# Performance work log

Measured on AMD Instinct MI355X. Metric: run time of the kernel, lower is better.

## Reference

```python
import jax, jax.numpy as jnp
import numpy as np

IN_DIM = 2048
OUT_DIM = 2048
GRID_SIZE = 8
BATCH = 4096
LN_EPS = 1e-5


def setup_inputs() -> dict:
    key = jax.random.key(0)
    k_x, k_w = jax.random.split(key)
    x = jax.random.normal(k_x, (BATCH, IN_DIM), dtype=jnp.float32)
    spline_weight = jax.random.normal(k_w, (OUT_DIM, IN_DIM, GRID_SIZE), dtype=jnp.float32) * 0.1
    return {
        "x": x,
        "ln_weight": jnp.ones((IN_DIM,), jnp.float32),
        "ln_bias": jnp.zeros((IN_DIM,), jnp.float32),
        "spline_weight": spline_weight,
        "scale_base": jnp.ones((OUT_DIM, IN_DIM), jnp.float32),
        "bias": jnp.zeros((OUT_DIM,), jnp.float32),
        "rbf_beta": jnp.full((1,), 2.0, jnp.float32),
        "grid": jnp.linspace(-1.0, 1.0, GRID_SIZE, dtype=jnp.float32),
    }


def reference(x, ln_weight, ln_bias, spline_weight, scale_base, bias, rbf_beta, grid):
    # LayerNorm over last dim (eps=1e-5, elementwise affine)
    mu = jnp.mean(x, axis=-1, keepdims=True)
    var = jnp.mean(jnp.square(x - mu), axis=-1, keepdims=True)
    xn = (x - mu) * jax.lax.rsqrt(var + LN_EPS) * ln_weight + ln_bias  # (B, in)

    beta = jnp.clip(rbf_beta, 0.5, 6.0)  # (1,)
    # RBF basis: (B, in, G)
    basis = jnp.exp(-jnp.square(xn[..., None] - grid) * beta)

    # Torch einsum('bdig,oid->bod') broadcasts the singleton d of basis against
    # spline_weight's last axis and sums g; after .sum(-1) this equals
    # (sum_g basis) @ (sum_d spline_weight).T
    S = basis.sum(-1)              # (B, in)
    Wd = spline_weight.sum(-1)     # (out, in)
    spline_sum = jnp.einsum('bi,oi->bo', S, Wd)

    base_out = jnp.einsum('bi,oi->bo', xn, scale_base)
    return base_out + spline_sum + bias
```

## Files before the change

kernel.cpp:

```cpp
#include <hip/hip_runtime.h>
#include <hip/hip_bf16.h>
#include <stdint.h>

constexpr int IN_DIM   = 2048;
constexpr int OUT_DIM  = 2048;
constexpr int BATCH    = 4096;
constexpr int KDIM     = 2 * IN_DIM;
constexpr float LN_EPS = 1e-5f;

#define TILE 128
#define BK   64
constexpr int NK    = KDIM / BK;
constexpr int STAGE = TILE * BK;

typedef __attribute__((ext_vector_type(8))) short  short8;
typedef __attribute__((ext_vector_type(4))) float  f32x4;

__device__ __forceinline__ unsigned short f2bf(float f) {
  __hip_bfloat16 h = __float2bfloat16(f);
  return *reinterpret_cast<unsigned short*>(&h);
}
__device__ __forceinline__ unsigned pack2bf(float a, float b) {
  return (unsigned)f2bf(a) | ((unsigned)f2bf(b) << 16);
}

__global__ __launch_bounds__(256) void ln_rbf_kernel(
    const float* __restrict__ x, const float* __restrict__ lnw,
    const float* __restrict__ lnb, const float* __restrict__ betap,
    const float* __restrict__ grid, unsigned short* __restrict__ A)
{
  const int row = blockIdx.x;
  const int tid = threadIdx.x;
  const float4* xr = reinterpret_cast<const float4*>(x + (size_t)row * IN_DIM);
  float4 v0 = xr[tid];
  float4 v1 = xr[tid + 256];
  float s = (v0.x + v0.y) + (v0.z + v0.w) + (v1.x + v1.y) + (v1.z + v1.w);
  float q = v0.x * v0.x + v0.y * v0.y + v0.z * v0.z + v0.w * v0.w
          + v1.x * v1.x + v1.y * v1.y + v1.z * v1.z + v1.w * v1.w;
  #pragma unroll
  for (int off = 32; off > 0; off >>= 1) {
    s += __shfl_down(s, off, 64);
    q += __shfl_down(q, off, 64);
  }
  __shared__ float red[10];
  const int lane = tid & 63, wv = tid >> 6;
  if (lane == 0) { red[wv] = s; red[4 + wv] = q; }
  __syncthreads();
  if (tid == 0) {
    float ts = (red[0] + red[1]) + (red[2] + red[3]);
    float tq = (red[4] + red[5]) + (red[6] + red[7]);
    float mu  = ts * (1.0f / IN_DIM);
    float var = tq * (1.0f / IN_DIM) - mu * mu;
    red[8] = mu;
    red[9] = rsqrtf(var + LN_EPS);
  }
  __syncthreads();
  const float mu = red[8], rs = red[9];
  const float beta = fminf(fmaxf(betap[0], 0.5f), 6.0f);
  float g[8];
  #pragma unroll
  for (int i = 0; i < 8; i++) g[i] = grid[i];
  const float4* w4 = reinterpret_cast<const float4*>(lnw);
  const float4* b4 = reinterpret_cast<const float4*>(lnb);
  unsigned short* Ar = A + (size_t)row * KDIM;
  #pragma unroll
  for (int h = 0; h < 2; h++) {
    const int idx = tid + h * 256;
    float4 xv  = (h == 0) ? v0 : v1;
    float4 wv4 = w4[idx];
    float4 bv4 = b4[idx];
    float xa[4] = {xv.x, xv.y, xv.z, xv.w};
    float wa[4] = {wv4.x, wv4.y, wv4.z, wv4.w};
    float ba[4] = {bv4.x, bv4.y, bv4.z, bv4.w};
    float xn[4], S[4];
    #pragma unroll
    for (int c = 0; c < 4; c++) {
      float xnv = (xa[c] - mu) * rs * wa[c] + ba[c];
      xn[c] = xnv;
      float acc = 0.f;
      #pragma unroll
      for (int gg = 0; gg < 8; gg++) {
        float d = xnv - g[gg];
        acc += __expf(-beta * d * d);
      }
      S[c] = acc;
    }
    uint2 px, ps;
    px.x = pack2bf(xn[0], xn[1]);
    px.y = pack2bf(xn[2], xn[3]);
    ps.x = pack2bf(S[0], S[1]);
    ps.y = pack2bf(S[2], S[3]);
    *reinterpret_cast<uint2*>(Ar + idx * 4) = px;
    *reinterpret_cast<uint2*>(Ar + IN_DIM + idx * 4) = ps;
  }
}

constexpr int SW_F4   = OUT_DIM * IN_DIM * 2;
constexpr int SB_F4   = OUT_DIM * IN_DIM / 4;

__global__ __launch_bounds__(256) void pack_b_kernel(
    const float* __restrict__ sw, const float* __restrict__ sb,
    unsigned* __restrict__ Bu)
{
  const int g = blockIdx.x * 256 + threadIdx.x;
  const int lane = threadIdx.x & 63;
  if (g < SW_F4) {
    float4 v = reinterpret_cast<const float4*>(sw)[g];
    float s = (v.x + v.y) + (v.z + v.w);
    s += __shfl_xor(s, 1, 64);
    float hi = __shfl_down(s, 2, 64);
    if ((lane & 3) == 0) {
      const int i_lin = g >> 1;
      const int o = i_lin >> 11;
      const int i = i_lin & (IN_DIM - 1);
      Bu[(size_t)o * (KDIM / 2) + (IN_DIM / 2) + (i >> 1)] = pack2bf(s, hi);
    }
  } else {
    const int t = g - SW_F4;
    float4 v = reinterpret_cast<const float4*>(sb)[t];
    const int o  = t >> 9;
    const int i4 = t & 511;
    uint2 u;
    u.x = pack2bf(v.x, v.y);
    u.y = pack2bf(v.z, v.w);
    *reinterpret_cast<uint2*>(&Bu[(size_t)o * (KDIM / 2) + i4 * 2]) = u;
  }
}

__device__ __forceinline__ void gld_lds16(const unsigned short* g, unsigned short* l) {
  __builtin_amdgcn_global_load_lds(
      (const __attribute__((address_space(1))) void*)g,
      (__attribute__((address_space(3))) void*)l, 16, 0, 0);
}

__global__ __launch_bounds__(256) void gemm_kernel(
    const unsigned short* __restrict__ A, const unsigned short* __restrict__ Bm,
    const float* __restrict__ bias, float* __restrict__ out)
{
  __shared__ __align__(16) unsigned short As[2 * STAGE];
  __shared__ __align__(16) unsigned short Bs[2 * STAGE];
  const int tid  = threadIdx.x;
  const int lane = tid & 63;
  const int wv   = tid >> 6;
  const int wr   = wv >> 1;
  const int wc   = wv & 1;
  const int m0   = blockIdx.y * TILE;
  const int n0   = blockIdx.x * TILE;
  const int lrow = lane & 15;
  const int lkq  = lane >> 4;

  f32x4 acc[4][4] = {};

  const unsigned short* Ap[4];
  const unsigned short* Bp[4];
  unsigned short* ldsA[4];
  unsigned short* ldsB[4];
  #pragma unroll
  for (int j = 0; j < 4; j++) {
    const int seg  = j * 256 + wv * 64 + lane;
    const int row  = seg >> 3;
    const int gcol = ((seg & 7) ^ (row & 7)) * 8;
    Ap[j] = A  + (size_t)(m0 + row) * KDIM + gcol;
    Bp[j] = Bm + (size_t)(n0 + row) * KDIM + gcol;
    ldsA[j] = &As[(j * 256 + wv * 64) * 8];
    ldsB[j] = &Bs[(j * 256 + wv * 64) * 8];
  }

  #pragma unroll
  for (int j = 0; j < 4; j++) gld_lds16(Ap[j], ldsA[j]);
  #pragma unroll
  for (int j = 0; j < 4; j++) gld_lds16(Bp[j], ldsB[j]);

  #pragma unroll 1
  for (int kt = 0; kt < NK; kt++) {
    __syncthreads();
    const int cur = (kt & 1) * STAGE;
    if (kt + 1 < NK) {
      const int nxt = ((kt + 1) & 1) * STAGE;
      const int koff = (kt + 1) * BK;
      #pragma unroll
      for (int j = 0; j < 4; j++) gld_lds16(Ap[j] + koff, ldsA[j] + nxt);
      #pragma unroll
      for (int j = 0; j < 4; j++) gld_lds16(Bp[j] + koff, ldsB[j] + nxt);
    }

    short8 af[2][4], bf[2][4];
    #pragma unroll
    for (int h = 0; h < 2; h++) {
      #pragma unroll
      for (int mi = 0; mi < 4; mi++) {
        const int r = wr * 64 + mi * 16 + lrow;
        af[h][mi] = *reinterpret_cast<const short8*>(
            &As[cur + r * BK + (((h << 2) | lkq) ^ (lrow & 7)) * 8]);
      }
      #pragma unroll
      for (int ni = 0; ni < 4; ni++) {
        const int r = wc * 64 + ni * 16 + lrow;
        bf[h][ni] = *reinterpret_cast<const short8*>(
            &Bs[cur + r * BK + (((h << 2) | lkq) ^ (lrow & 7)) * 8]);
      }
    }
    #pragma unroll
    for (int h = 0; h < 2; h++)
      #pragma unroll
      for (int mi = 0; mi < 4; mi++)
        #pragma unroll
        for (int ni = 0; ni < 4; ni++)
          acc[mi][ni] = __builtin_amdgcn_mfma_f32_16x16x32_bf16(
              af[h][mi], bf[h][ni], acc[mi][ni], 0, 0, 0);
  }

  const int rb = (lane >> 4) * 4;
  #pragma unroll
  for (int ni = 0; ni < 4; ni++) {
    const int col = n0 + wc * 64 + ni * 16 + lrow;
    const float bv = bias[col];
    #pragma unroll
    for (int mi = 0; mi < 4; mi++) {
      const int rowm = m0 + wr * 64 + mi * 16 + rb;
      #pragma unroll
      for (int r = 0; r < 4; r++)
        out[(size_t)(rowm + r) * OUT_DIM + col] = acc[mi][ni][r] + bv;
    }
  }
}

extern "C" void kernel_launch(void* const* d_in, const int* in_sizes, int n_in,
                              void* d_out, int out_size, void* d_ws, size_t ws_size,
                              hipStream_t stream) {
  const float* x    = (const float*)d_in[0];
  const float* lnw  = (const float*)d_in[1];
  const float* lnb  = (const float*)d_in[2];
  const float* sw   = (const float*)d_in[3];
  const float* sb   = (const float*)d_in[4];
  const float* bias = (const float*)d_in[5];
  const float* beta = (const float*)d_in[6];
  const float* grid = (const float*)d_in[7];
  float* out = (float*)d_out;

  unsigned short* A = (unsigned short*)d_ws;
  unsigned short* B = A + (size_t)BATCH * KDIM;

  hipLaunchKernelGGL(ln_rbf_kernel, dim3(BATCH), dim3(256), 0, stream,
                     x, lnw, lnb, beta, grid, A);
  hipLaunchKernelGGL(pack_b_kernel, dim3((SW_F4 + SB_F4) / 256), dim3(256), 0, stream,
                     sw, sb, (unsigned*)B);
  hipLaunchKernelGGL(gemm_kernel, dim3(OUT_DIM / TILE, BATCH / TILE), dim3(256), 0, stream,
                     A, B, bias, out);
}
```

Measured before the change: 311.9 us.

## Split GEMM into producer and consumer waves synchronised through LDS atomic counters

```diff
diff --git a/kernel.cpp b/kernel.cpp
--- a/kernel.cpp
+++ b/kernel.cpp
@@ -133,56 +133,75 @@
       (__attribute__((address_space(3))) void*)l, 16, 0, 0);
 }
 
-__global__ __launch_bounds__(256) void gemm_kernel(
+__global__ __launch_bounds__(512) void gemm_kernel(
     const unsigned short* __restrict__ A, const unsigned short* __restrict__ Bm,
     const float* __restrict__ bias, float* __restrict__ out)
 {
   __shared__ __align__(16) unsigned short As[2 * STAGE];
   __shared__ __align__(16) unsigned short Bs[2 * STAGE];
+  __shared__ unsigned prod_done, cons_done;
+
   const int tid  = threadIdx.x;
   const int lane = tid & 63;
   const int wv   = tid >> 6;
+  const int m0   = blockIdx.y * TILE;
+  const int n0   = blockIdx.x * TILE;
+
+  if (tid == 0) { prod_done = 0u; cons_done = 0u; }
+  __syncthreads();
+
+  if (wv >= 4) {
+    const int p = wv - 4;
+    const unsigned short* Ap[4];
+    const unsigned short* Bp[4];
+    unsigned short* lA[4];
+    unsigned short* lB[4];
+    #pragma unroll
+    for (int j = 0; j < 4; j++) {
+      const int seg  = j * 256 + p * 64 + lane;
+      const int row  = seg >> 3;
+      const int gcol = ((seg & 7) ^ (row & 7)) * 8;
+      Ap[j] = A  + (size_t)(m0 + row) * KDIM + gcol;
+      Bp[j] = Bm + (size_t)(n0 + row) * KDIM + gcol;
+      lA[j] = &As[(j * 256 + p * 64) * 8];
+      lB[j] = &Bs[(j * 256 + p * 64) * 8];
+    }
+    #pragma unroll 1
+    for (int kt = 0; kt < NK; kt++) {
+      if (kt >= 2) {
+        const unsigned need = 4u * (unsigned)(kt - 1);
+        while (__hip_atomic_load(&cons_done, __ATOMIC_ACQUIRE,
+                                 __HIP_MEMORY_SCOPE_WORKGROUP) < need)
+          __builtin_amdgcn_s_sleep(1);
+      }
+      const int slot = (kt & 1) * STAGE;
+      const int koff = kt * BK;
+      #pragma unroll
+      for (int j = 0; j < 4; j++) gld_lds16(Ap[j] + koff, lA[j] + slot);
+      #pragma unroll
+      for (int j = 0; j < 4; j++) gld_lds16(Bp[j] + koff, lB[j] + slot);
+      __builtin_amdgcn_s_waitcnt(0);
+      if (lane == 0)
+        __hip_atomic_fetch_add(&prod_done, 1u, __ATOMIC_RELEASE,
+                               __HIP_MEMORY_SCOPE_WORKGROUP);
+    }
+    return;
+  }
+
   const int wr   = wv >> 1;
   const int wc   = wv & 1;
-  const int m0   = blockIdx.y * TILE;
-  const int n0   = blockIdx.x * TILE;
   const int lrow = lane & 15;
   const int lkq  = lane >> 4;
 
   f32x4 acc[4][4] = {};
 
-  const unsigned short* Ap[4];
-  const unsigned short* Bp[4];
-  unsigned short* ldsA[4];
-  unsigned short* ldsB[4];
-  #pragma unroll
-  for (int j = 0; j < 4; j++) {
-    const int seg  = j * 256 + wv * 64 + lane;
-    const int row  = seg >> 3;
-    const int gcol = ((seg & 7) ^ (row & 7)) * 8;
-    Ap[j] = A  + (size_t)(m0 + row) * KDIM + gcol;
-    Bp[j] = Bm + (size_t)(n0 + row) * KDIM + gcol;
-    ldsA[j] = &As[(j * 256 + wv * 64) * 8];
-    ldsB[j] = &Bs[(j * 256 + wv * 64) * 8];
-  }
-
-  #pragma unroll
-  for (int j = 0; j < 4; j++) gld_lds16(Ap[j], ldsA[j]);
-  #pragma unroll
-  for (int j = 0; j < 4; j++) gld_lds16(Bp[j], ldsB[j]);
-
   #pragma unroll 1
   for (int kt = 0; kt < NK; kt++) {
-    __syncthreads();
+    const unsigned need = 4u * (unsigned)(kt + 1);
+    while (__hip_atomic_load(&prod_done, __ATOMIC_ACQUIRE,
+                             __HIP_MEMORY_SCOPE_WORKGROUP) < need)
+      __builtin_amdgcn_s_sleep(1);
     const int cur = (kt & 1) * STAGE;
-    if (kt + 1 < NK) {
-      const int nxt = ((kt + 1) & 1) * STAGE;
-      const int koff = (kt + 1) * BK;
-      #pragma unroll
-      for (int j = 0; j < 4; j++) gld_lds16(Ap[j] + koff, ldsA[j] + nxt);
-      #pragma unroll
-      for (int j = 0; j < 4; j++) gld_lds16(Bp[j] + koff, ldsB[j] + nxt);
-    }
 
     short8 af[2][4], bf[2][4];
     #pragma unroll
@@ -208,6 +227,10 @@
         for (int ni = 0; ni < 4; ni++)
           acc[mi][ni] = __builtin_amdgcn_mfma_f32_16x16x32_bf16(
               af[h][mi], bf[h][ni], acc[mi][ni], 0, 0, 0);
+
+    if (lane == 0)
+      __hip_atomic_fetch_add(&cons_done, 1u, __ATOMIC_RELEASE,
+                             __HIP_MEMORY_SCOPE_WORKGROUP);
   }
 
   const int rb = (lane >> 4) * 4;
@@ -245,6 +268,6 @@
                      x, lnw, lnb, beta, grid, A);
   hipLaunchKernelGGL(pack_b_kernel, dim3((SW_F4 + SB_F4) / 256), dim3(256), 0, stream,
                      sw, sb, (unsigned*)B);
-  hipLaunchKernelGGL(gemm_kernel, dim3(OUT_DIM / TILE, BATCH / TILE), dim3(256), 0, stream,
+  hipLaunchKernelGGL(gemm_kernel, dim3(OUT_DIM / TILE, BATCH / TILE), dim3(512), 0, stream,
                      A, B, bias, out);
 }
```

Measured after the change: 312.1 us. About the same (+0.1%).
